# Kernel optimization log

Hardware: AMD Instinct MI355X
Metric: run time of the kernel (lower is better)

## Reference

```python
import jax, jax.numpy as jnp
import numpy as np


def _normalize_adj(edge_index, num_nodes):
    # add self loops
    loop = jnp.arange(num_nodes, dtype=edge_index.dtype)
    row = jnp.concatenate([edge_index[0], loop])
    col = jnp.concatenate([edge_index[1], loop])
    deg = jax.ops.segment_sum(jnp.ones(row.shape[0], jnp.float32), row,
                              num_segments=num_nodes)
    dis = jnp.where(deg > 0, jax.lax.rsqrt(deg), 0.0)  # deg^{-1/2}, inf->0
    ew = dis[row] * dis[col]
    return row, col, ew


def _gcn_conv(x, W, b, row, col, ew, num_nodes):
    h = x @ W.T + b                       # dense linear [N, out]
    msg = h[col] * ew[:, None]            # gather + scale [E', out]
    return jax.ops.segment_sum(msg, row, num_segments=num_nodes)  # scatter_add


def setup_inputs() -> dict:
    N, E, IN, HID, OUT = 100000, 1600000, 128, 128, 64
    key = jax.random.key(0)
    k1, k2, k3, k4 = jax.random.split(key, 4)
    x = jax.random.normal(k1, (N, IN), jnp.float32)
    edge_index = jax.random.randint(k2, (2, E), 0, N, jnp.int64)
    # xavier_uniform for weights, zero bias (as in reset_parameters)
    lim1 = float(np.sqrt(6.0 / (IN + HID)))
    lim2 = float(np.sqrt(6.0 / (HID + OUT)))
    W1 = jax.random.uniform(k3, (HID, IN), jnp.float32, -lim1, lim1)
    b1 = jnp.zeros((HID,), jnp.float32)
    W2 = jax.random.uniform(k4, (OUT, HID), jnp.float32, -lim2, lim2)
    b2 = jnp.zeros((OUT,), jnp.float32)
    return {"x": x, "edge_index": edge_index, "num_nodes": N,
            "W1": W1, "b1": b1, "W2": W2, "b2": b2}


def reference(x, edge_index, num_nodes, W1, b1, W2, b2):
    row, col, ew = _normalize_adj(edge_index, num_nodes)
    h = _gcn_conv(x, W1, b1, row, col, ew, num_nodes)
    h = jax.nn.relu(h)  # dropout is identity in eval mode
    out = _gcn_conv(h, W2, b2, row, col, ew, num_nodes)
    return out
```

## Files before the change

kernel.cpp:

```cpp
#include <hip/hip_runtime.h>
#include <hip/hip_bf16.h>
#include <stdint.h>


#define TPB 256
#define NBLK_C 256
#define TPB_C 1024
#define MAX_NB 2048

typedef __attribute__((ext_vector_type(8))) __bf16 bf16x8;
typedef __attribute__((ext_vector_type(4))) float f32x4;
typedef __attribute__((ext_vector_type(2))) float f32x2;

__device__ __forceinline__ float bf16lo(unsigned u) { return __uint_as_float(u << 16); }
__device__ __forceinline__ float bf16hi(unsigned u) { return __uint_as_float(u & 0xffff0000u); }
__device__ __forceinline__ unsigned short f2bf(float f) {
    unsigned u = __float_as_uint(f);
    return (unsigned short)((u + 0x7fff + ((u >> 16) & 1)) >> 16);
}
__device__ __forceinline__ f32x2 pk_add(f32x2 a, f32x2 b) {
    f32x2 d;
    asm("v_pk_add_f32 %0, %1, %2" : "=v"(d) : "v"(a), "v"(b));
    return d;
}

__global__ __launch_bounds__(TPB_C) void hist_extract_kernel(const void* __restrict__ ei, int E,
                                                             int CH,
                                                             int* __restrict__ row32,
                                                             int* __restrict__ col32,
                                                             int* __restrict__ hist,
                                                             int NB, int N) {
    __shared__ int h[MAX_NB];
    __shared__ int s_is64;
    int tid = threadIdx.x;
    if (tid < 64) {
        int x = ((const int*)ei)[2 * tid + 1];
        unsigned long long b = __ballot(x != 0);
        if (tid == 0) s_is64 = (b == 0ull);
    }
    for (int bin = tid; bin < NB; bin += TPB_C) h[bin] = 0;
    __syncthreads();

    int b = blockIdx.x;
    int s = b * CH;
    int end = min(E, s + CH);
    int is64 = s_is64;
    unsigned uN = (unsigned)N;
    if (is64) {
        const long long* p = (const long long*)ei;
        for (int e = s + tid; e < end; e += TPB_C) {
            int r = (int)p[e];
            int c = (int)p[E + e];
            row32[e] = r;
            col32[e] = c;
            if ((unsigned)r < uN && (unsigned)c < uN) atomicAdd(&h[r >> 7], 1);
        }
    } else {
        const int* p = (const int*)ei;
        for (int e = s + tid; e < end; e += TPB_C) {
            int r = p[e];
            int c = p[E + e];
            row32[e] = r;
            col32[e] = c;
            if ((unsigned)r < uN && (unsigned)c < uN) atomicAdd(&h[r >> 7], 1);
        }
    }
    __syncthreads();
    for (int bin = tid; bin < NB; bin += TPB_C) hist[bin * NBLK_C + b] = h[bin];
}

__global__ __launch_bounds__(NBLK_C) void colscan_kernel(int* __restrict__ hist,
                                                         int* __restrict__ binTotal) {
    __shared__ int sm[NBLK_C];
    int bin = blockIdx.x;
    int tid = threadIdx.x;
    int v = hist[bin * NBLK_C + tid];
    sm[tid] = v;
    __syncthreads();
    for (int o = 1; o < NBLK_C; o <<= 1) {
        int x = (tid >= o) ? sm[tid - o] : 0;
        __syncthreads();
        sm[tid] += x;
        __syncthreads();
    }
    hist[bin * NBLK_C + tid] = sm[tid] - v;
    if (tid == NBLK_C - 1) binTotal[bin] = sm[NBLK_C - 1];
}

__global__ __launch_bounds__(TPB_C) void scatter_kernel(const int* __restrict__ row32,
                                                        const int* __restrict__ col32, int E,
                                                        int CH,
                                                        const int* __restrict__ hist,
                                                        const int* __restrict__ binTotal,
                                                        int* __restrict__ bucketed,
                                                        int NB, int N) {
    __shared__ int cur[MAX_NB];
    __shared__ int sm2[TPB_C];
    int tid = threadIdx.x;
    int b = blockIdx.x;

    int v = (tid < NB) ? binTotal[tid] : 0;
    sm2[tid] = v;
    __syncthreads();
    for (int o = 1; o < TPB_C; o <<= 1) {
        int x = (tid >= o) ? sm2[tid - o] : 0;
        __syncthreads();
        sm2[tid] += x;
        __syncthreads();
    }
    if (tid < NB) cur[tid] = (sm2[tid] - v) + hist[tid * NBLK_C + b];
    __syncthreads();

    int s = b * CH;
    int end = min(E, s + CH);
    unsigned uN = (unsigned)N;
    for (int e = s + tid; e < end; e += TPB_C) {
        int r = row32[e];
        int c = col32[e];
        if ((unsigned)r < uN && (unsigned)c < uN) {
            int pos = atomicAdd(&cur[r >> 7], 1);
            bucketed[pos] = (c << 7) | (r & 127);
        }
    }
}

__global__ __launch_bounds__(TPB) void finecsr_kernel(const int* __restrict__ bucketed,
                                                      const int* __restrict__ binTotal,
                                                      int4* __restrict__ meta,
                                                      float* __restrict__ dis,
                                                      int* __restrict__ csr, int N) {
    __shared__ int c128[128];
    __shared__ int cur128[128];
    __shared__ int sm[TPB];
    __shared__ int red[TPB];
    int bin = blockIdx.x;
    int tid = threadIdx.x;

    int part = 0;
    for (int i = tid; i < bin; i += TPB) part += binTotal[i];
    red[tid] = part;
    __syncthreads();
    for (int o = TPB / 2; o > 0; o >>= 1) {
        if (tid < o) red[tid] += red[tid + o];
        __syncthreads();
    }
    int s = red[0];
    int m = binTotal[bin];

    if (tid < 128) c128[tid] = 0;
    __syncthreads();
    for (int i = tid; i < m; i += TPB) atomicAdd(&c128[bucketed[s + i] & 127], 1);
    __syncthreads();

    int v = (tid < 128) ? c128[tid] : 0;
    sm[tid] = v;
    __syncthreads();
    for (int o = 1; o < 128; o <<= 1) {
        int x = (tid >= o) ? sm[tid - o] : 0;
        __syncthreads();
        sm[tid] += x;
        __syncthreads();
    }
    if (tid < 128) {
        int excl = sm[tid] - v;
        int r = bin * 128 + tid;
        if (r < N) {
            float dv = rsqrtf((float)v + 1.0f);
            meta[r] = make_int4(s + excl, v, __float_as_int(dv), 0);
            dis[r] = dv;
        }
        cur128[tid] = s + excl;
    }
    __syncthreads();
    for (int i = tid; i < m; i += TPB) {
        int p = bucketed[s + i];
        int pos = atomicAdd(&cur128[p & 127], 1);
        csr[pos] = p >> 7;
    }
}

template <int BN, bool INB16>
__global__ __launch_bounds__(256, 2) void gemm_mfma_kernel(const void* __restrict__ Xp,
                                                           const float* __restrict__ W,
                                                           const float* __restrict__ bias,
                                                           const float* __restrict__ dis,
                                                           unsigned short* __restrict__ Hb,
                                                           int N) {
    constexpr int XST = 136;
    __shared__ unsigned short Xs[128 * XST];
    __shared__ unsigned short Ws[BN * XST];

    const int tid = threadIdx.x;
    const int r0 = blockIdx.x * 128;

    if (blockIdx.x == 0 && tid < (BN >> 1))
        ((unsigned*)Hb)[(size_t)N * (BN >> 1) + tid] = 0u;

    if (INB16) {
        const ushort4* Xv = (const ushort4*)Xp;
        for (int idx = tid; idx < 128 * 32; idx += 256) {
            int row = idx >> 5, q = idx & 31;
            int rg = r0 + row;
            if (rg >= N) rg = N - 1;
            *(ushort4*)&Xs[row * XST + q * 4] = Xv[(size_t)rg * 32 + q];
        }
    } else {
        const float4* Xv = (const float4*)Xp;
        for (int idx = tid; idx < 128 * 32; idx += 256) {
            int row = idx >> 5, q = idx & 31;
            int rg = r0 + row;
            if (rg >= N) rg = N - 1;
            float4 v = Xv[(size_t)rg * 32 + q];
            ushort4 s = make_ushort4(f2bf(v.x), f2bf(v.y), f2bf(v.z), f2bf(v.w));
            *(ushort4*)&Xs[row * XST + q * 4] = s;
        }
    }
    {
        const float4* Wv = (const float4*)W;
        for (int idx = tid; idx < BN * 32; idx += 256) {
            int n = idx >> 5, q = idx & 31;
            float4 v = Wv[n * 32 + q];
            ushort4 s = make_ushort4(f2bf(v.x), f2bf(v.y), f2bf(v.z), f2bf(v.w));
            *(ushort4*)&Ws[n * XST + q * 4] = s;
        }
    }
    __syncthreads();

    constexpr int RT = (BN == 128) ? 4 : 2;
    constexpr int CT = 4;
    const int wave = tid >> 6, lane = tid & 63;
    const int l15 = lane & 15, q8 = lane >> 4;
    const int row0 = (BN == 128) ? (wave & 1) * 64 : wave * 32;
    const int col0 = (BN == 128) ? (wave >> 1) * 64 : 0;

    f32x4 zero = {0.f, 0.f, 0.f, 0.f};
    f32x4 acc[RT][CT];
#pragma unroll
    for (int rt = 0; rt < RT; ++rt)
#pragma unroll
        for (int ct = 0; ct < CT; ++ct) acc[rt][ct] = zero;

#pragma unroll
    for (int ks = 0; ks < 4; ++ks) {
        int ko = ks * 32 + q8 * 8;
        bf16x8 a[RT], b[CT];
#pragma unroll
        for (int rt = 0; rt < RT; ++rt)
            a[rt] = *(const bf16x8*)&Xs[(row0 + rt * 16 + l15) * XST + ko];
#pragma unroll
        for (int ct = 0; ct < CT; ++ct)
            b[ct] = *(const bf16x8*)&Ws[(col0 + ct * 16 + l15) * XST + ko];
#pragma unroll
        for (int rt = 0; rt < RT; ++rt)
#pragma unroll
            for (int ct = 0; ct < CT; ++ct)
                acc[rt][ct] = __builtin_amdgcn_mfma_f32_16x16x32_bf16(
                    a[rt], b[ct], acc[rt][ct], 0, 0, 0);
    }

    float bv[CT];
#pragma unroll
    for (int ct = 0; ct < CT; ++ct) bv[ct] = bias[col0 + ct * 16 + l15];
#pragma unroll
    for (int rt = 0; rt < RT; ++rt)
#pragma unroll
        for (int r = 0; r < 4; ++r) {
            int row = r0 + row0 + rt * 16 + q8 * 4 + r;
            if (row < N) {
                float dn = dis[row];
#pragma unroll
                for (int ct = 0; ct < CT; ++ct)
                    Hb[(size_t)row * BN + col0 + ct * 16 + l15] =
                        f2bf((acc[rt][ct][r] + bv[ct]) * dn);
            }
        }
}

template <int F, bool RELU, bool OB16>
__global__ __launch_bounds__(TPB) void agg_kernel(const unsigned short* __restrict__ Hb,
                                                  const int* __restrict__ csr,
                                                  const int4* __restrict__ meta,
                                                  void* __restrict__ outp, int N) {
    constexpr int FPL = F / 16;
    constexpr int NW = FPL / 2;
    constexpr int RS = F / 2;

    const int lane = threadIdx.x & 63;
    const int g = lane >> 4;
    const int fl = lane & 15;
    const int W = gridDim.x << 2;

    int w = (blockIdx.x << 2) + (threadIdx.x >> 6);
    if (w >= N) return;

    const unsigned* Hu = (const unsigned*)Hb;

    auto load_row = [&](unsigned (&u)[NW], int r) {
        if constexpr (NW == 4) {
            uint4 v = *(const uint4*)(Hu + (size_t)r * RS + fl * NW);
            u[0] = v.x; u[1] = v.y; u[2] = v.z; u[3] = v.w;
        } else {
            uint2 v = *(const uint2*)(Hu + (size_t)r * RS + fl * NW);
            u[0] = v.x; u[1] = v.y;
        }
    };

    int4 m = meta[w];
    int s = m.x, d = m.y;
    float di = __int_as_float(m.z);
    int cl = (lane < d) ? csr[s + lane] : 0;

    while (true) {
        const int wn = w + W;
        const bool has_next = wn < N;
        int sn = 0, dn = 0, cln = 0;
        float din = 0.f;
        if (has_next) {
            int4 mn = meta[wn];
            sn = mn.x; dn = mn.y; din = __int_as_float(mn.z);
            cln = (lane < dn) ? csr[sn + lane] : 0;
        }

        f32x2 acc2[NW];
#pragma unroll
        for (int t = 0; t < NW; ++t) acc2[t] = (f32x2){0.f, 0.f};

        auto accum_row = [&](const unsigned (&u)[NW]) {
#pragma unroll
            for (int t = 0; t < NW; ++t) {
                f32x2 lh;
                lh.x = bf16lo(u[t]);
                lh.y = bf16hi(u[t]);
                acc2[t] = pk_add(acc2[t], lh);
            }
        };

        if (g == 0) {
            unsigned su[NW];
            load_row(su, w);
            accum_row(su);
        }

        int clc = cl;
        for (int base = 0; base < d; base += 64) {
            int rem = d - base;
            if (rem > 64) rem = 64;
            if (base > 0) clc = (lane < rem) ? csr[s + base + lane] : 0;

            for (int e = 0; e < rem; e += 32) {
                int cc0[4];
#pragma unroll
                for (int k = 0; k < 4; ++k) {
                    int idx = e + k * 4 + g;
                    int raw = __shfl(clc, idx & 63);
                    cc0[k] = (idx < rem) ? raw : N;
                }
                unsigned u0[4][NW];
#pragma unroll
                for (int k = 0; k < 4; ++k) load_row(u0[k], cc0[k]);

                const bool two = (e + 16) < rem;
                int cc1[4];
                unsigned u1[4][NW];
                if (two) {
#pragma unroll
                    for (int k = 0; k < 4; ++k) {
                        int idx = e + 16 + k * 4 + g;
                        int raw = __shfl(clc, idx & 63);
                        cc1[k] = (idx < rem) ? raw : N;
                    }
#pragma unroll
                    for (int k = 0; k < 4; ++k) load_row(u1[k], cc1[k]);
                }
#pragma unroll
                for (int k = 0; k < 4; ++k) accum_row(u0[k]);
                if (two) {
#pragma unroll
                    for (int k = 0; k < 4; ++k) accum_row(u1[k]);
                }
            }
        }

#pragma unroll
        for (int off = 16; off < 64; off <<= 1)
#pragma unroll
            for (int t = 0; t < NW; ++t) {
                acc2[t].x += __shfl_xor(acc2[t].x, off);
                acc2[t].y += __shfl_xor(acc2[t].y, off);
            }

#pragma unroll
        for (int t = 0; t < NW; ++t) {
            acc2[t].x *= di;
            acc2[t].y *= di;
            if (RELU) {
                acc2[t].x = fmaxf(acc2[t].x, 0.0f);
                acc2[t].y = fmaxf(acc2[t].y, 0.0f);
            }
        }

        if (lane < 16) {
            if constexpr (OB16) {
                unsigned dw[NW];
#pragma unroll
                for (int t = 0; t < NW; ++t)
                    dw[t] = (unsigned)f2bf(acc2[t].x) | ((unsigned)f2bf(acc2[t].y) << 16);
                unsigned* op = (unsigned*)outp;
                if constexpr (NW == 4) {
                    *(uint4*)&op[(size_t)w * RS + fl * NW] =
                        make_uint4(dw[0], dw[1], dw[2], dw[3]);
                } else {
                    *(uint2*)&op[(size_t)w * RS + fl * NW] = make_uint2(dw[0], dw[1]);
                }
            } else {
                float4* op = (float4*)outp;
                if constexpr (NW == 2) {
                    op[(size_t)w * 16 + fl] =
                        make_float4(acc2[0].x, acc2[0].y, acc2[1].x, acc2[1].y);
                } else {
                    op[(size_t)w * 32 + fl * 2] =
                        make_float4(acc2[0].x, acc2[0].y, acc2[1].x, acc2[1].y);
                    op[(size_t)w * 32 + fl * 2 + 1] =
                        make_float4(acc2[2].x, acc2[2].y, acc2[3].x, acc2[3].y);
                }
            }
        }

        if (!has_next) break;
        w = wn; s = sn; d = dn; di = din; cl = cln;
    }
}

extern "C" void kernel_launch(void* const* d_in, const int* in_sizes, int n_in,
                              void* d_out, int out_size, void* d_ws, size_t ws_size,
                              hipStream_t stream) {
    const float* x  = (const float*)d_in[0];
    const void*  ei = d_in[1];
    const float* W1 = (const float*)d_in[3];
    const float* b1 = (const float*)d_in[4];
    const float* W2 = (const float*)d_in[5];
    const float* b2 = (const float*)d_in[6];
    float* out = (float*)d_out;

    const int IN = 128, HID = 128;
    const int N = in_sizes[0] / IN;
    const int E = in_sizes[1] / 2;
    const int NB = (N + 127) >> 7;
    const int CH = (E + NBLK_C - 1) / NBLK_C;

    char* ws = (char*)d_ws;
    size_t off = 0;
    auto alloc = [&](size_t bytes) -> void* {
        void* p = (void*)(ws + off);
        off += (bytes + 255) & ~(size_t)255;
        return p;
    };
    int4*  meta     = (int4*)alloc((size_t)N * 16);
    float* dis      = (float*)alloc((size_t)N * 4);
    int*   row32    = (int*)alloc((size_t)E * 4);
    int*   col32    = (int*)alloc((size_t)E * 4);
    int*   bucketed = (int*)alloc((size_t)E * 4);
    int*   csr      = (int*)alloc((size_t)E * 4);
    int*   hist     = (int*)alloc((size_t)NB * NBLK_C * 4);
    int*   binTotal = (int*)alloc((size_t)NB * 4);
    unsigned short* H1b = (unsigned short*)alloc((size_t)(N + 1) * HID * 2);
    unsigned short* R1b = (unsigned short*)alloc((size_t)(N + 1) * HID * 2);
    unsigned short* H2b = H1b;

    hist_extract_kernel<<<NBLK_C, TPB_C, 0, stream>>>(ei, E, CH, row32, col32,
                                                      hist, NB, N);
    colscan_kernel<<<NB, NBLK_C, 0, stream>>>(hist, binTotal);
    scatter_kernel<<<NBLK_C, TPB_C, 0, stream>>>(row32, col32, E, CH, hist, binTotal,
                                                 bucketed, NB, N);
    finecsr_kernel<<<NB, TPB, 0, stream>>>(bucketed, binTotal, meta, dis, csr, N);

    int ngrid = (N + 127) / 128;
    int agrid = (N + 3) / 4;
    if (agrid > 2048) agrid = 2048;

    gemm_mfma_kernel<128, false><<<ngrid, 256, 0, stream>>>(x, W1, b1, dis, H1b, N);
    agg_kernel<128, true, true><<<agrid, TPB, 0, stream>>>(H1b, csr, meta, R1b, N);

    gemm_mfma_kernel<64, true><<<ngrid, 256, 0, stream>>>(R1b, W2, b2, dis, H2b, N);
    agg_kernel<64, false, false><<<agrid, TPB, 0, stream>>>(H2b, csr, meta, out, N);
}
```

Measured before the change: 291.1 us.

## Launch one wavefront per node in aggregation with width-adaptive lane groups

Replaces the persistent grid-stride aggregation loop, which prefetched the next node's metadata, with a full grid of one wavefront per node. For the 64-feature layer, each lane now loads 16 bytes and more edge groups run in parallel. Index loads and output stores use nontemporal hints. This removes the cross-node prefetch overlap in favour of more resident waves, so latency hiding now relies on occupancy, and it adds block scheduling cost for about 25k blocks.

```diff
diff --git a/kernel.cpp b/kernel.cpp
--- a/kernel.cpp
+++ b/kernel.cpp
@@ -11,6 +11,7 @@
 typedef __attribute__((ext_vector_type(8))) __bf16 bf16x8;
 typedef __attribute__((ext_vector_type(4))) float f32x4;
 typedef __attribute__((ext_vector_type(2))) float f32x2;
+typedef __attribute__((ext_vector_type(4))) unsigned int u32x4;
 
 __device__ __forceinline__ float bf16lo(unsigned u) { return __uint_as_float(u << 16); }
 __device__ __forceinline__ float bf16hi(unsigned u) { return __uint_as_float(u & 0xffff0000u); }
@@ -281,153 +282,120 @@
                                                   const int* __restrict__ csr,
                                                   const int4* __restrict__ meta,
                                                   void* __restrict__ outp, int N) {
-    constexpr int FPL = F / 16;
-    constexpr int NW = FPL / 2;
     constexpr int RS = F / 2;
-
+    constexpr int LPR = RS / 4;
+    constexpr int G = 64 / LPR;
+    constexpr int NW = 4;
+
+    int w = (blockIdx.x * TPB + threadIdx.x) >> 6;
+    if (w >= N) return;
     const int lane = threadIdx.x & 63;
-    const int g = lane >> 4;
-    const int fl = lane & 15;
-    const int W = gridDim.x << 2;
-
-    int w = (blockIdx.x << 2) + (threadIdx.x >> 6);
-    if (w >= N) return;
+    const int g = lane / LPR;
+    const int fl = lane % LPR;
+
+    int4 m = meta[w];
+    const int s = m.x, d = m.y;
+    const float di = __int_as_float(m.z);
 
     const unsigned* Hu = (const unsigned*)Hb;
 
+    f32x2 acc2[NW];
+#pragma unroll
+    for (int t = 0; t < NW; ++t) acc2[t] = (f32x2){0.f, 0.f};
+
+    auto accum_row = [&](const unsigned (&u)[NW]) {
+#pragma unroll
+        for (int t = 0; t < NW; ++t) {
+            f32x2 lh;
+            lh.x = bf16lo(u[t]);
+            lh.y = bf16hi(u[t]);
+            acc2[t] = pk_add(acc2[t], lh);
+        }
+    };
     auto load_row = [&](unsigned (&u)[NW], int r) {
-        if constexpr (NW == 4) {
-            uint4 v = *(const uint4*)(Hu + (size_t)r * RS + fl * NW);
-            u[0] = v.x; u[1] = v.y; u[2] = v.z; u[3] = v.w;
+        u32x4 v = *(const u32x4*)(Hu + (size_t)r * RS + fl * NW);
+        u[0] = v.x; u[1] = v.y; u[2] = v.z; u[3] = v.w;
+    };
+
+    if (g == 0) {
+        unsigned su[NW];
+        load_row(su, w);
+        accum_row(su);
+    }
+
+    for (int base = 0; base < d; base += 64) {
+        int rem = d - base;
+        if (rem > 64) rem = 64;
+        int cl = (lane < rem) ? __builtin_nontemporal_load(csr + s + base + lane) : 0;
+
+        for (int e = 0; e < rem; e += 8 * G) {
+            int cc0[4];
+#pragma unroll
+            for (int k = 0; k < 4; ++k) {
+                int idx = e + k * G + g;
+                int raw = __shfl(cl, idx & 63);
+                cc0[k] = (idx < rem) ? raw : N;
+            }
+            unsigned u0[4][NW];
+#pragma unroll
+            for (int k = 0; k < 4; ++k) load_row(u0[k], cc0[k]);
+
+            const bool two = (e + 4 * G) < rem;
+            int cc1[4];
+            unsigned u1[4][NW];
+            if (two) {
+#pragma unroll
+                for (int k = 0; k < 4; ++k) {
+                    int idx = e + 4 * G + k * G + g;
+                    int raw = __shfl(cl, idx & 63);
+                    cc1[k] = (idx < rem) ? raw : N;
+                }
+#pragma unroll
+                for (int k = 0; k < 4; ++k) load_row(u1[k], cc1[k]);
+            }
+#pragma unroll
+            for (int k = 0; k < 4; ++k) accum_row(u0[k]);
+            if (two) {
+#pragma unroll
+                for (int k = 0; k < 4; ++k) accum_row(u1[k]);
+            }
+        }
+    }
+
+#pragma unroll
+    for (int off = LPR; off < 64; off <<= 1)
+#pragma unroll
+        for (int t = 0; t < NW; ++t) {
+            acc2[t].x += __shfl_xor(acc2[t].x, off);
+            acc2[t].y += __shfl_xor(acc2[t].y, off);
+        }
+
+#pragma unroll
+    for (int t = 0; t < NW; ++t) {
+        acc2[t].x *= di;
+        acc2[t].y *= di;
+        if (RELU) {
+            acc2[t].x = fmaxf(acc2[t].x, 0.0f);
+            acc2[t].y = fmaxf(acc2[t].y, 0.0f);
+        }
+    }
+
+    if (lane < LPR) {
+        if constexpr (OB16) {
+            u32x4 dw;
+            dw.x = (unsigned)f2bf(acc2[0].x) | ((unsigned)f2bf(acc2[0].y) << 16);
+            dw.y = (unsigned)f2bf(acc2[1].x) | ((unsigned)f2bf(acc2[1].y) << 16);
+            dw.z = (unsigned)f2bf(acc2[2].x) | ((unsigned)f2bf(acc2[2].y) << 16);
+            dw.w = (unsigned)f2bf(acc2[3].x) | ((unsigned)f2bf(acc2[3].y) << 16);
+            unsigned* op = (unsigned*)outp;
+            __builtin_nontemporal_store(dw, (u32x4*)(op + (size_t)w * RS + fl * NW));
         } else {
-            uint2 v = *(const uint2*)(Hu + (size_t)r * RS + fl * NW);
-            u[0] = v.x; u[1] = v.y;
-        }
-    };
-
-    int4 m = meta[w];
-    int s = m.x, d = m.y;
-    float di = __int_as_float(m.z);
-    int cl = (lane < d) ? csr[s + lane] : 0;
-
-    while (true) {
-        const int wn = w + W;
-        const bool has_next = wn < N;
-        int sn = 0, dn = 0, cln = 0;
-        float din = 0.f;
-        if (has_next) {
-            int4 mn = meta[wn];
-            sn = mn.x; dn = mn.y; din = __int_as_float(mn.z);
-            cln = (lane < dn) ? csr[sn + lane] : 0;
-        }
-
-        f32x2 acc2[NW];
-#pragma unroll
-        for (int t = 0; t < NW; ++t) acc2[t] = (f32x2){0.f, 0.f};
-
-        auto accum_row = [&](const unsigned (&u)[NW]) {
-#pragma unroll
-            for (int t = 0; t < NW; ++t) {
-                f32x2 lh;
-                lh.x = bf16lo(u[t]);
-                lh.y = bf16hi(u[t]);
-                acc2[t] = pk_add(acc2[t], lh);
-            }
-        };
-
-        if (g == 0) {
-            unsigned su[NW];
-            load_row(su, w);
-            accum_row(su);
-        }
-
-        int clc = cl;
-        for (int base = 0; base < d; base += 64) {
-            int rem = d - base;
-            if (rem > 64) rem = 64;
-            if (base > 0) clc = (lane < rem) ? csr[s + base + lane] : 0;
-
-            for (int e = 0; e < rem; e += 32) {
-                int cc0[4];
-#pragma unroll
-                for (int k = 0; k < 4; ++k) {
-                    int idx = e + k * 4 + g;
-                    int raw = __shfl(clc, idx & 63);
-                    cc0[k] = (idx < rem) ? raw : N;
-                }
-                unsigned u0[4][NW];
-#pragma unroll
-                for (int k = 0; k < 4; ++k) load_row(u0[k], cc0[k]);
-
-                const bool two = (e + 16) < rem;
-                int cc1[4];
-                unsigned u1[4][NW];
-                if (two) {
-#pragma unroll
-                    for (int k = 0; k < 4; ++k) {
-                        int idx = e + 16 + k * 4 + g;
-                        int raw = __shfl(clc, idx & 63);
-                        cc1[k] = (idx < rem) ? raw : N;
-                    }
-#pragma unroll
-                    for (int k = 0; k < 4; ++k) load_row(u1[k], cc1[k]);
-                }
-#pragma unroll
-                for (int k = 0; k < 4; ++k) accum_row(u0[k]);
-                if (two) {
-#pragma unroll
-                    for (int k = 0; k < 4; ++k) accum_row(u1[k]);
-                }
-            }
-        }
-
-#pragma unroll
-        for (int off = 16; off < 64; off <<= 1)
-#pragma unroll
-            for (int t = 0; t < NW; ++t) {
-                acc2[t].x += __shfl_xor(acc2[t].x, off);
-                acc2[t].y += __shfl_xor(acc2[t].y, off);
-            }
-
-#pragma unroll
-        for (int t = 0; t < NW; ++t) {
-            acc2[t].x *= di;
-            acc2[t].y *= di;
-            if (RELU) {
-                acc2[t].x = fmaxf(acc2[t].x, 0.0f);
-                acc2[t].y = fmaxf(acc2[t].y, 0.0f);
-            }
-        }
-
-        if (lane < 16) {
-            if constexpr (OB16) {
-                unsigned dw[NW];
-#pragma unroll
-                for (int t = 0; t < NW; ++t)
-                    dw[t] = (unsigned)f2bf(acc2[t].x) | ((unsigned)f2bf(acc2[t].y) << 16);
-                unsigned* op = (unsigned*)outp;
-                if constexpr (NW == 4) {
-                    *(uint4*)&op[(size_t)w * RS + fl * NW] =
-                        make_uint4(dw[0], dw[1], dw[2], dw[3]);
-                } else {
-                    *(uint2*)&op[(size_t)w * RS + fl * NW] = make_uint2(dw[0], dw[1]);
-                }
-            } else {
-                float4* op = (float4*)outp;
-                if constexpr (NW == 2) {
-                    op[(size_t)w * 16 + fl] =
-                        make_float4(acc2[0].x, acc2[0].y, acc2[1].x, acc2[1].y);
-                } else {
-                    op[(size_t)w * 32 + fl * 2] =
-                        make_float4(acc2[0].x, acc2[0].y, acc2[1].x, acc2[1].y);
-                    op[(size_t)w * 32 + fl * 2 + 1] =
-                        make_float4(acc2[2].x, acc2[2].y, acc2[3].x, acc2[3].y);
-                }
-            }
-        }
-
-        if (!has_next) break;
-        w = wn; s = sn; d = dn; di = din; cl = cln;
+            f32x4 v0 = {acc2[0].x, acc2[0].y, acc2[1].x, acc2[1].y};
+            f32x4 v1 = {acc2[2].x, acc2[2].y, acc2[3].x, acc2[3].y};
+            f32x4* op = (f32x4*)outp;
+            __builtin_nontemporal_store(v0, op + (size_t)w * (F / 4) + fl * 2);
+            __builtin_nontemporal_store(v1, op + (size_t)w * (F / 4) + fl * 2 + 1);
+        }
     }
 }
 
@@ -476,7 +444,6 @@
 
     int ngrid = (N + 127) / 128;
     int agrid = (N + 3) / 4;
-    if (agrid > 2048) agrid = 2048;
 
     gemm_mfma_kernel<128, false><<<ngrid, 256, 0, stream>>>(x, W1, b1, dis, H1b, N);
     agg_kernel<128, true, true><<<agrid, TPB, 0, stream>>>(H1b, csr, meta, R1b, N);
```

New measurement: 292.0 us. About the same (+0.3%).
